# Performance work log

Measured on AMD Instinct MI355X. Metric: run time of the kernel, lower is better.

## Reference

```python
import jax, jax.numpy as jnp
import numpy as np

NUM_HEADS = 12

def setup_inputs() -> dict:
    key = jax.random.key(0)
    k1, k2, k3 = jax.random.split(key, 3)
    B, T, H = 2, 2048, 768
    x = jax.random.normal(k1, (B, T, H), dtype=jnp.float32)
    attn_mask = jnp.ones((B, T), dtype=jnp.int32)
    Wqkv = jax.random.normal(k2, (H, 3 * H), dtype=jnp.float32) * 0.02
    bqkv = jnp.zeros((3 * H,), dtype=jnp.float32)
    Wproj = jax.random.normal(k3, (H, H), dtype=jnp.float32) * 0.02
    bproj = jnp.zeros((H,), dtype=jnp.float32)
    return {"x": x, "attn_mask": attn_mask, "Wqkv": Wqkv, "bqkv": bqkv,
            "Wproj": Wproj, "bproj": bproj}

def reference(x, attn_mask, Wqkv, bqkv, Wproj, bproj):
    B, T, H = x.shape
    nh = NUM_HEADS
    hd = H // nh
    qkv = x @ Wqkv + bqkv                      # [B,T,3H]
    q, k, v = jnp.split(qkv, 3, axis=-1)
    # [B,T,H] -> [B,nh,T,hd]
    def heads(t):
        return t.reshape(B, T, nh, hd).transpose(0, 2, 1, 3)
    q, k, v = heads(q), heads(k), heads(v)
    scores = jnp.einsum('bhqd,bhkd->bhqk', q, k) / jnp.sqrt(jnp.float32(hd))
    causal = jnp.tril(jnp.ones((T, T), dtype=bool))          # allowed positions
    key_ok = attn_mask.astype(bool)[:, None, None, :]        # [B,1,1,T]
    allowed = causal[None, None] & key_ok
    scores = jnp.where(allowed, scores, -jnp.inf)
    weights = jax.nn.softmax(scores, axis=-1)                # dropout=0 (eval)
    out = jnp.einsum('bhqk,bhkd->bhqd', weights, v)
    out = out.transpose(0, 2, 1, 3).reshape(B, T, H)
    return out @ Wproj + bproj
```

## Files before the change

### kernel.cpp

```cpp
#include <hip/hip_runtime.h>
#include <stdint.h>

typedef unsigned short u16;
typedef unsigned int   u32;
typedef unsigned char  u8;
typedef __attribute__((ext_vector_type(8))) short short8;
typedef __attribute__((ext_vector_type(4))) float f32x4;
typedef __attribute__((ext_vector_type(4))) unsigned short u16x4;
typedef __attribute__((ext_vector_type(4))) unsigned int u32x4;

#define DEV static __device__ __forceinline__

static constexpr int Bc = 2, Tc = 2048, Hc = 768, NH = 12, HD = 64;
static constexpr int BTc = Bc * Tc;
static constexpr int N3 = 3 * Hc;
static constexpr int NBH = Bc * NH;
static constexpr int NITEMS = 32 * NBH;
static constexpr float QSCALE = 0.125f * 1.44269504088896f;
static constexpr float MRINIT = -1.0e38f;
static constexpr float SMASK  = -3.0e38f;

DEV u16 f2bf(float f) {
  u32 u = __float_as_uint(f);
  u32 r = (u + 0x7fffu + ((u >> 16) & 1u)) >> 16;
  return (u16)r;
}

DEV float fexp2(float x) {
#if __has_builtin(__builtin_amdgcn_exp2f)
  return __builtin_amdgcn_exp2f(x);
#else
  return exp2f(x);
#endif
}

DEV u32 cvtpk_bf16(float lo, float hi) {
  u32 r;
  asm("v_cvt_pk_bf16_f32 %0, %1, %2" : "=v"(r) : "v"(lo), "v"(hi));
  return r;
}

DEV void gl_lds16(const u16* g, u16* l) {
  __builtin_amdgcn_global_load_lds(
      (const __attribute__((address_space(1))) u32*)g,
      (__attribute__((address_space(3))) u32*)l, 16, 0, 0);
}

#define MFMA(a, b, c) __builtin_amdgcn_mfma_f32_16x16x32_bf16((a), (b), (c), 0, 0, 0)

__global__ void k_cvt(const float4* __restrict__ in, uint4* __restrict__ out, int n8,
                      const int* __restrict__ mask, u8* __restrict__ flags,
                      u32* __restrict__ ctr) {
  if (blockIdx.x == 0 && threadIdx.x < 64) {
    int t = threadIdx.x;
    if (t == 0) *ctr = 0;
    int b = t >> 5, kb = t & 31;
    const int* m = mask + b * Tc + kb * 64;
    int all = 1;
    for (int i = 0; i < 64; ++i) all &= (m[i] != 0);
    flags[b * 32 + kb] = (u8)all;
  }
  int i = blockIdx.x * 256 + threadIdx.x;
  if (i >= n8) return;
  float4 a = in[2 * i], b = in[2 * i + 1];
  uint4 o;
  o.x = f2bf(a.x) | ((u32)f2bf(a.y) << 16);
  o.y = f2bf(a.z) | ((u32)f2bf(a.w) << 16);
  o.z = f2bf(b.x) | ((u32)f2bf(b.y) << 16);
  o.w = f2bf(b.z) | ((u32)f2bf(b.w) << 16);
  out[i] = o;
}

__global__ __launch_bounds__(256) void k_transpose_w2(const float* __restrict__ Wqkv,
                                                      const float* __restrict__ Wproj,
                                                      u16* __restrict__ WqkvT,
                                                      u16* __restrict__ WprojT) {
  __shared__ u16 tile[64][65];
  int y = blockIdx.y, x = blockIdx.x;
  const float* in; u16* out; int R, C, r0, c0;
  if (y < 12) { in = Wqkv; out = WqkvT; R = Hc; C = N3; r0 = y * 64; c0 = x * 64; }
  else {
    if (x >= 12) return;
    in = Wproj; out = WprojT; R = Hc; C = Hc; r0 = (y - 12) * 64; c0 = x * 64;
  }
  int tx = threadIdx.x, ty = threadIdx.y;
  for (int i = ty; i < 64; i += 4)
    tile[i][tx] = f2bf(in[(size_t)(r0 + i) * C + c0 + tx]);
  __syncthreads();
  for (int i = ty; i < 64; i += 4)
    out[(size_t)(c0 + i) * R + r0 + tx] = tile[tx][i];
}

template <int EPI>
__global__ __launch_bounds__(256) void k_gemm(const u16* __restrict__ A,
                                              const u16* __restrict__ BTm,
                                              const float* __restrict__ bias,
                                              u16* __restrict__ oQ, u16* __restrict__ oK,
                                              u16* __restrict__ oV, float* __restrict__ oF,
                                              int M, int N, int K) {
  __shared__ u16 As[128 * 32];
  __shared__ u16 Bs[128 * 32];
  const int tid = threadIdx.x;
  const int lane = tid & 63, wave = tid >> 6;
  const int wr = wave >> 1, wc = wave & 1;
  const int row0 = blockIdx.y * 128, col0 = blockIdx.x * 128;

  f32x4 acc[4][4];
#pragma unroll
  for (int m = 0; m < 4; ++m)
#pragma unroll
    for (int n = 0; n < 4; ++n) acc[m][n] = (f32x4)(0.f);

  const int srow = lane >> 2;
  const int sg = lane & 3;
  const int sf = (lane >> 3) & 3;
  const int kfetch = ((sg ^ sf) * 8);

  const int r16 = lane & 15;
  const int g = lane >> 4;
  const int fr = (r16 >> 1) & 3;
  const int koff = ((g ^ fr) * 8);

  for (int k0 = 0; k0 < K; k0 += 32) {
    if (k0) __syncthreads();
#pragma unroll
    for (int p = 0; p < 2; ++p) {
      int seg = wave * 2 + p;
      int row = seg * 16 + srow;
      gl_lds16(A + (size_t)(row0 + row) * K + k0 + kfetch, &As[seg * 512 + lane * 8]);
      gl_lds16(BTm + (size_t)(col0 + row) * K + k0 + kfetch, &Bs[seg * 512 + lane * 8]);
    }
    __syncthreads();
    short8 af[4], bf[4];
#pragma unroll
    for (int m = 0; m < 4; ++m)
      af[m] = *(const short8*)&As[(wr * 64 + m * 16 + r16) * 32 + koff];
#pragma unroll
    for (int n = 0; n < 4; ++n)
      bf[n] = *(const short8*)&Bs[(wc * 64 + n * 16 + r16) * 32 + koff];
#pragma unroll
    for (int m = 0; m < 4; ++m)
#pragma unroll
      for (int n = 0; n < 4; ++n)
        acc[m][n] = MFMA(af[m], bf[n], acc[m][n]);
  }

#pragma unroll
  for (int m = 0; m < 4; ++m) {
    int rowg = row0 + wr * 64 + m * 16 + g * 4;
#pragma unroll
    for (int n = 0; n < 4; ++n) {
      int colg = col0 + wc * 64 + n * 16 + r16;
      float bv = bias[colg];
      if constexpr (EPI == 0) {
        int which = colg / Hc;
        int hc = colg - which * Hc;
        int h = hc >> 6, d = hc & 63;
        int b = rowg >> 11, t0 = rowg & 2047;
        if (which == 2) {
          int o = t0 & 31;
          int t0p = (t0 & ~31) | (((o >> 2) & 3) * 8 + ((o >> 4) & 1) * 4);
          u16x4 pk;
#pragma unroll
          for (int r = 0; r < 4; ++r) pk[r] = f2bf(acc[m][n][r] + bv);
          *(u16x4*)&oV[((size_t)(b * NH + h) * HD + d) * Tc + t0p] = pk;
        } else {
#pragma unroll
          for (int r = 0; r < 4; ++r) {
            float v = acc[m][n][r] + bv;
            size_t dst = ((size_t)(b * NH + h) * Tc + t0 + r) * HD + d;
            if (which == 0) oQ[dst] = f2bf(v * QSCALE);
            else            oK[dst] = f2bf(v);
          }
        }
      } else {
#pragma unroll
        for (int r = 0; r < 4; ++r)
          oF[(size_t)(rowg + r) * Hc + colg] = acc[m][n][r] + bv;
      }
    }
  }
}

__global__ __launch_bounds__(512, 4) void k_attn(const u16* __restrict__ Qh,
                                                 const u16* __restrict__ Kh,
                                                 const u16* __restrict__ VT,
                                                 const int* __restrict__ mask,
                                                 const u8* __restrict__ flags,
                                                 u16* __restrict__ O,
                                                 u32* __restrict__ ctr) {
  __shared__ u16 Ks[4][4096];
  __shared__ u16 Vs[4][4096];
  __shared__ float mlb[128];
  __shared__ int s_item;
  const int tid = threadIdx.x, lane = tid & 63, wave = tid >> 6;
  const int qgrp = wave >> 1;
  const int kh = wave & 1;
  const int r16 = lane & 15, g = lane >> 4;
  const int r7 = r16 & 7;
  const int skey = lane >> 3;
  const int sgr = lane & 7;
  const int sgd = ((sgr ^ skey) * 8);

  const int off0 = r16 * 64 + ((g ^ r7) * 8);
  const int off1 = r16 * 64 + (((4 + g) ^ r7) * 8);
  const int offv = kh ? off1 : off0;

  for (;;) {
    if (tid == 0) s_item = (int)atomicAdd(ctr, 1u);
    __syncthreads();
    const int item = s_item;
    if (item >= NITEMS) break;
    const int qt = 31 - item / NBH;
    const int bh = item % NBH;
    const int b = bh / NH, h = bh - b * NH;
    const int q0 = qt * 64;
    const int nt = qt + 1;
    const int qg = q0 + qgrp * 16 + r16;
    const int* mrow = mask + b * Tc;
    const u8* frow = flags + b * 32;

    const u16* qbase = Qh + ((size_t)bh * Tc + qg) * HD;
    const short8 qf0 = *(const short8*)(qbase + g * 8);
    const short8 qf1 = *(const short8*)(qbase + 32 + g * 8);

    f32x4 acc[4];
#pragma unroll
    for (int n = 0; n < 4; ++n) acc[n] = (f32x4)(0.f);
    float mrun = MRINIT, lrun = 0.f;

    const u16* kgb = Kh + (size_t)bh * Tc * HD;
    const u16* vgb = VT + (size_t)bh * HD * Tc;

    auto stage = [&](int slot, int kb) {
      int rloc = wave * 8 + skey;
      gl_lds16(kgb + (size_t)(kb + rloc) * HD + sgd, &Ks[slot][wave * 512 + lane * 8]);
      gl_lds16(vgb + (size_t)rloc * Tc + kb + sgd, &Vs[slot][wave * 512 + lane * 8]);
    };

    f32x4 sP0, sP1;
    auto process = [&](int u, f32x4 s0, f32x4 s1) {
      const int kbw = 64 * u + 32 * kh;
      const bool diag = (u == nt - 1);
      if (diag || !frow[u]) {
        const int fl = frow[u];
#pragma unroll
        for (int np = 0; np < 2; ++np)
#pragma unroll
          for (int r = 0; r < 4; ++r) {
            int keyg = kbw + 16 * np + 4 * g + r;
            bool ok = fl ? true : (mrow[keyg] != 0);
            if (diag) ok = ok && (keyg <= qg);
            if (!ok) { if (np == 0) s0[r] = SMASK; else s1[r] = SMASK; }
          }
      }
      float lm = fmaxf(fmaxf(fmaxf(s0[0], s0[1]), fmaxf(s0[2], s0[3])),
                       fmaxf(fmaxf(s1[0], s1[1]), fmaxf(s1[2], s1[3])));
      if (!__all(lm <= mrun + 8.0f)) {
        float rm = fmaxf(lm, __shfl_xor(lm, 16));
        rm = fmaxf(rm, __shfl_xor(rm, 32));
        float nm = fmaxf(mrun, rm);
        float alpha = fexp2(mrun - nm);
        mrun = nm;
        lrun *= alpha;
#pragma unroll
        for (int r = 0; r < 4; ++r) {
          float ar = __shfl(alpha, g * 4 + r);
          acc[0][r] *= ar; acc[1][r] *= ar; acc[2][r] *= ar; acc[3][r] *= ar;
        }
      }
      float p0[4], p1[4];
#pragma unroll
      for (int r = 0; r < 4; ++r) {
        p0[r] = fexp2(s0[r] - mrun);
        p1[r] = fexp2(s1[r] - mrun);
      }
      lrun += ((p0[0] + p0[1]) + (p0[2] + p0[3])) + ((p1[0] + p1[1]) + (p1[2] + p1[3]));
      u32x4 PL;
      PL[0] = cvtpk_bf16(p0[0], p0[1]); PL[1] = cvtpk_bf16(p0[2], p0[3]);
      PL[2] = cvtpk_bf16(p1[0], p1[1]); PL[3] = cvtpk_bf16(p1[2], p1[3]);
      short8 pa = __builtin_bit_cast(short8, PL);
      const u16* Vc = &Vs[u & 3][0];
      __builtin_amdgcn_s_setprio(1);
#pragma unroll
      for (int n = 0; n < 4; ++n) {
        short8 vf = *(const short8*)&Vc[n * 1024 + offv];
        acc[n] = MFMA(pa, vf, acc[n]);
      }
      __builtin_amdgcn_s_setprio(0);
    };

    stage(0, 0);
    if (nt > 1) stage(1, 64);

    for (int t = 0; t < nt; ++t) {
      const int kb = t * 64;
      const int rem = nt - 1 - t;

      if (rem >= 1) asm volatile("s_waitcnt vmcnt(2)" ::: "memory");
      else          asm volatile("s_waitcnt vmcnt(0)" ::: "memory");
      __builtin_amdgcn_sched_barrier(0);
      __builtin_amdgcn_s_barrier();
      __builtin_amdgcn_sched_barrier(0);

      if (rem >= 2) stage((t + 2) & 3, kb + 128);

      const u16* Kc = &Ks[t & 3][0];
      f32x4 sN0, sN1;
      __builtin_amdgcn_s_setprio(1);
      {
        const int ng = 2 * kh;
        short8 kf0 = *(const short8*)&Kc[ng * 1024 + off0];
        short8 kf1 = *(const short8*)&Kc[ng * 1024 + off1];
        f32x4 z = (f32x4)(0.f);
        z = MFMA(kf0, qf0, z); z = MFMA(kf1, qf1, z);
        sN0 = z;
        short8 kf2 = *(const short8*)&Kc[(ng + 1) * 1024 + off0];
        short8 kf3 = *(const short8*)&Kc[(ng + 1) * 1024 + off1];
        f32x4 w = (f32x4)(0.f);
        w = MFMA(kf2, qf0, w); w = MFMA(kf3, qf1, w);
        sN1 = w;
      }
      __builtin_amdgcn_s_setprio(0);

      if (t > 0) process(t - 1, sP0, sP1);
      sP0 = sN0; sP1 = sN1;
    }
    process(nt - 1, sP0, sP1);

    float lt = lrun + __shfl_xor(lrun, 16);
    lt += __shfl_xor(lt, 32);

    __syncthreads();
    float* ab = (float*)&Ks[0][0] + qgrp * 1024;
    if (kh == 1) {
#pragma unroll
      for (int n = 0; n < 4; ++n)
#pragma unroll
        for (int r = 0; r < 4; ++r)
          ab[(4 * g + r) * 64 + 16 * n + r16] = acc[n][r];
      if (g == 0) {
        mlb[qgrp * 32 + r16 * 2]     = mrun;
        mlb[qgrp * 32 + r16 * 2 + 1] = lt;
      }
    }
    __syncthreads();
    if (kh == 0) {
#pragma unroll
      for (int r = 0; r < 4; ++r) {
        int q = 4 * g + r;
        float mA = __shfl(mrun, q);
        float lA = __shfl(lt, q);
        float mB = mlb[qgrp * 32 + q * 2];
        float lB = mlb[qgrp * 32 + q * 2 + 1];
        float ms = fmaxf(mA, mB);
        float cA = fexp2(mA - ms);
        float cB = fexp2(mB - ms);
        float linv = 1.0f / (lA * cA + lB * cB);
        int qr = q0 + qgrp * 16 + q;
        u16* orow = O + ((size_t)(b * Tc + qr)) * Hc + h * 64;
#pragma unroll
        for (int n = 0; n < 4; ++n) {
          float v = (acc[n][r] * cA + ab[q * 64 + 16 * n + r16] * cB) * linv;
          orow[n * 16 + r16] = f2bf(v);
        }
      }
    }
  }
}

extern "C" void kernel_launch(void* const* d_in, const int* in_sizes, int n_in,
                              void* d_out, int out_size, void* d_ws, size_t ws_size,
                              hipStream_t stream) {
  const float* x = (const float*)d_in[0];
  const int* mask = (const int*)d_in[1];
  const float* Wqkv = (const float*)d_in[2];
  const float* bqkv = (const float*)d_in[3];
  const float* Wproj = (const float*)d_in[4];
  const float* bproj = (const float*)d_in[5];
  float* out = (float*)d_out;

  char* ws = (char*)d_ws;
  size_t off = 0;
  auto alloc = [&](size_t bytes) {
    char* p = ws + off;
    off += (bytes + 255) & ~(size_t)255;
    return p;
  };
  u16* xb     = (u16*)alloc((size_t)BTc * Hc * 2);
  u16* WqkvT  = (u16*)alloc((size_t)N3 * Hc * 2);
  u16* WprojT = (u16*)alloc((size_t)Hc * Hc * 2);
  u16* Qh     = (u16*)alloc((size_t)BTc * Hc * 2);
  u16* Kh     = (u16*)alloc((size_t)BTc * Hc * 2);
  u16* VT     = (u16*)alloc((size_t)BTc * Hc * 2);
  u32* ctr    = (u32*)alloc(256);
  u8*  flags  = (u8*)alloc(256);
  u16* Ob     = xb;

  int n8 = BTc * Hc / 8;
  k_cvt<<<(n8 + 255) / 256, 256, 0, stream>>>((const float4*)x, (uint4*)xb, n8,
                                              mask, flags, ctr);
  k_transpose_w2<<<dim3(36, 24), dim3(64, 4), 0, stream>>>(Wqkv, Wproj, WqkvT, WprojT);
  k_gemm<0><<<dim3(N3 / 128, BTc / 128), 256, 0, stream>>>(xb, WqkvT, bqkv, Qh, Kh, VT,
                                                           nullptr, BTc, N3, Hc);
  k_attn<<<dim3(512), 512, 0, stream>>>(Qh, Kh, VT, mask, flags, Ob, ctr);
  k_gemm<1><<<dim3(Hc / 128, BTc / 128), 256, 0, stream>>>(Ob, WprojT, bproj, nullptr,
                                                           nullptr, nullptr, out, BTc, Hc, Hc);
}
```

Baseline: 103.6 us.

## Triple-buffer GEMM loads with XCD swizzle; simplify attention to double-buffered loop

The GEMM kernel gains a three-slot LDS ring with prefetch two K-steps ahead and a single barrier per step, replacing the load/sync/compute loop. It also remaps workgroup IDs in an XCD-aware interleave to improve L2 locality. The attention kernel drops its software-pipelined QK/PV overlap and four-slot K/V ring in favour of a simpler two-slot loop with a full vmcnt(0) wait, removes the setprio hints, and launches NITEMS blocks instead of 512. This cuts attention LDS use, which may raise occupancy, but loses the overlap of QK^T with softmax/PV and exposes load latency.

After: 106.7 us. +3.0%, slower.

```diff
diff --git a/kernel.cpp b/kernel.cpp
--- a/kernel.cpp
+++ b/kernel.cpp
@@ -98,12 +98,17 @@
                                               u16* __restrict__ oQ, u16* __restrict__ oK,
                                               u16* __restrict__ oV, float* __restrict__ oF,
                                               int M, int N, int K) {
-  __shared__ u16 As[128 * 32];
-  __shared__ u16 Bs[128 * 32];
+  __shared__ u16 As[3][4096];
+  __shared__ u16 Bs[3][4096];
   const int tid = threadIdx.x;
   const int lane = tid & 63, wave = tid >> 6;
   const int wr = wave >> 1, wc = wave & 1;
-  const int row0 = blockIdx.y * 128, col0 = blockIdx.x * 128;
+
+  const int gx = gridDim.x;
+  const int nwg = gx * gridDim.y;
+  const int lin = blockIdx.y * gx + blockIdx.x;
+  const int wg = (lin & 7) * (nwg >> 3) + (lin >> 3);
+  const int row0 = (wg / gx) * 128, col0 = (wg % gx) * 128;
 
   f32x4 acc[4][4];
 #pragma unroll
@@ -121,23 +126,37 @@
   const int fr = (r16 >> 1) & 3;
   const int koff = ((g ^ fr) * 8);
 
-  for (int k0 = 0; k0 < K; k0 += 32) {
-    if (k0) __syncthreads();
+  auto stageG = [&](int slot, int k0) {
 #pragma unroll
     for (int p = 0; p < 2; ++p) {
       int seg = wave * 2 + p;
       int row = seg * 16 + srow;
-      gl_lds16(A + (size_t)(row0 + row) * K + k0 + kfetch, &As[seg * 512 + lane * 8]);
-      gl_lds16(BTm + (size_t)(col0 + row) * K + k0 + kfetch, &Bs[seg * 512 + lane * 8]);
+      gl_lds16(A + (size_t)(row0 + row) * K + k0 + kfetch, &As[slot][seg * 512 + lane * 8]);
+      gl_lds16(BTm + (size_t)(col0 + row) * K + k0 + kfetch, &Bs[slot][seg * 512 + lane * 8]);
     }
-    __syncthreads();
+  };
+
+  const int nk = K >> 5;
+  stageG(0, 0);
+  if (nk > 1) stageG(1, 32);
+
+  for (int kt = 0; kt < nk; ++kt) {
+    if (kt + 1 < nk) asm volatile("s_waitcnt vmcnt(4)" ::: "memory");
+    else             asm volatile("s_waitcnt vmcnt(0)" ::: "memory");
+    __builtin_amdgcn_sched_barrier(0);
+    __builtin_amdgcn_s_barrier();
+    __builtin_amdgcn_sched_barrier(0);
+    if (kt + 2 < nk) stageG((kt + 2) % 3, (kt + 2) * 32);
+
+    const u16* Ac = &As[kt % 3][0];
+    const u16* Bcur = &Bs[kt % 3][0];
     short8 af[4], bf[4];
 #pragma unroll
     for (int m = 0; m < 4; ++m)
-      af[m] = *(const short8*)&As[(wr * 64 + m * 16 + r16) * 32 + koff];
+      af[m] = *(const short8*)&Ac[(wr * 64 + m * 16 + r16) * 32 + koff];
 #pragma unroll
     for (int n = 0; n < 4; ++n)
-      bf[n] = *(const short8*)&Bs[(wc * 64 + n * 16 + r16) * 32 + koff];
+      bf[n] = *(const short8*)&Bcur[(wc * 64 + n * 16 + r16) * 32 + koff];
 #pragma unroll
     for (int m = 0; m < 4; ++m)
 #pragma unroll
@@ -189,8 +208,8 @@
                                                  const u8* __restrict__ flags,
                                                  u16* __restrict__ O,
                                                  u32* __restrict__ ctr) {
-  __shared__ u16 Ks[4][4096];
-  __shared__ u16 Vs[4][4096];
+  __shared__ u16 Ks[2][4096];
+  __shared__ u16 Vs[2][4096];
   __shared__ float mlb[128];
   __shared__ int s_item;
   const int tid = threadIdx.x, lane = tid & 63, wave = tid >> 6;
@@ -238,12 +257,40 @@
       gl_lds16(vgb + (size_t)rloc * Tc + kb + sgd, &Vs[slot][wave * 512 + lane * 8]);
     };
 
-    f32x4 sP0, sP1;
-    auto process = [&](int u, f32x4 s0, f32x4 s1) {
-      const int kbw = 64 * u + 32 * kh;
-      const bool diag = (u == nt - 1);
-      if (diag || !frow[u]) {
-        const int fl = frow[u];
+    stage(0, 0);
+
+    for (int t = 0; t < nt; ++t) {
+      const int kb = t * 64;
+
+      asm volatile("s_waitcnt vmcnt(0)" ::: "memory");
+      __builtin_amdgcn_sched_barrier(0);
+      __builtin_amdgcn_s_barrier();
+      __builtin_amdgcn_sched_barrier(0);
+
+      if (t + 1 < nt) stage((t + 1) & 1, kb + 64);
+
+      const u16* Kc = &Ks[t & 1][0];
+      const u16* Vc = &Vs[t & 1][0];
+
+      f32x4 s0, s1;
+      {
+        const int ng = 2 * kh;
+        short8 kf0 = *(const short8*)&Kc[ng * 1024 + off0];
+        short8 kf1 = *(const short8*)&Kc[ng * 1024 + off1];
+        f32x4 z = (f32x4)(0.f);
+        z = MFMA(kf0, qf0, z); z = MFMA(kf1, qf1, z);
+        s0 = z;
+        short8 kf2 = *(const short8*)&Kc[(ng + 1) * 1024 + off0];
+        short8 kf3 = *(const short8*)&Kc[(ng + 1) * 1024 + off1];
+        f32x4 w = (f32x4)(0.f);
+        w = MFMA(kf2, qf0, w); w = MFMA(kf3, qf1, w);
+        s1 = w;
+      }
+
+      const int kbw = kb + 32 * kh;
+      const bool diag = (t == nt - 1);
+      if (diag || !frow[t]) {
+        const int fl = frow[t];
 #pragma unroll
         for (int np = 0; np < 2; ++np)
 #pragma unroll
@@ -254,6 +301,7 @@
             if (!ok) { if (np == 0) s0[r] = SMASK; else s1[r] = SMASK; }
           }
       }
+
       float lm = fmaxf(fmaxf(fmaxf(s0[0], s0[1]), fmaxf(s0[2], s0[3])),
                        fmaxf(fmaxf(s1[0], s1[1]), fmaxf(s1[2], s1[3])));
       if (!__all(lm <= mrun + 8.0f)) {
@@ -276,57 +324,18 @@
         p1[r] = fexp2(s1[r] - mrun);
       }
       lrun += ((p0[0] + p0[1]) + (p0[2] + p0[3])) + ((p1[0] + p1[1]) + (p1[2] + p1[3]));
+
       u32x4 PL;
       PL[0] = cvtpk_bf16(p0[0], p0[1]); PL[1] = cvtpk_bf16(p0[2], p0[3]);
       PL[2] = cvtpk_bf16(p1[0], p1[1]); PL[3] = cvtpk_bf16(p1[2], p1[3]);
       short8 pa = __builtin_bit_cast(short8, PL);
-      const u16* Vc = &Vs[u & 3][0];
-      __builtin_amdgcn_s_setprio(1);
 #pragma unroll
       for (int n = 0; n < 4; ++n) {
         short8 vf = *(const short8*)&Vc[n * 1024 + offv];
         acc[n] = MFMA(pa, vf, acc[n]);
       }
-      __builtin_amdgcn_s_setprio(0);
-    };
-
-    stage(0, 0);
-    if (nt > 1) stage(1, 64);
-
-    for (int t = 0; t < nt; ++t) {
-      const int kb = t * 64;
-      const int rem = nt - 1 - t;
-
-      if (rem >= 1) asm volatile("s_waitcnt vmcnt(2)" ::: "memory");
-      else          asm volatile("s_waitcnt vmcnt(0)" ::: "memory");
       __builtin_amdgcn_sched_barrier(0);
-      __builtin_amdgcn_s_barrier();
-      __builtin_amdgcn_sched_barrier(0);
-
-      if (rem >= 2) stage((t + 2) & 3, kb + 128);
-
-      const u16* Kc = &Ks[t & 3][0];
-      f32x4 sN0, sN1;
-      __builtin_amdgcn_s_setprio(1);
-      {
-        const int ng = 2 * kh;
-        short8 kf0 = *(const short8*)&Kc[ng * 1024 + off0];
-        short8 kf1 = *(const short8*)&Kc[ng * 1024 + off1];
-        f32x4 z = (f32x4)(0.f);
-        z = MFMA(kf0, qf0, z); z = MFMA(kf1, qf1, z);
-        sN0 = z;
-        short8 kf2 = *(const short8*)&Kc[(ng + 1) * 1024 + off0];
-        short8 kf3 = *(const short8*)&Kc[(ng + 1) * 1024 + off1];
-        f32x4 w = (f32x4)(0.f);
-        w = MFMA(kf2, qf0, w); w = MFMA(kf3, qf1, w);
-        sN1 = w;
-      }
-      __builtin_amdgcn_s_setprio(0);
-
-      if (t > 0) process(t - 1, sP0, sP1);
-      sP0 = sN0; sP1 = sN1;
     }
-    process(nt - 1, sP0, sP1);
 
     float lt = lrun + __shfl_xor(lrun, 16);
     lt += __shfl_xor(lt, 32);
@@ -403,7 +412,7 @@
   k_transpose_w2<<<dim3(36, 24), dim3(64, 4), 0, stream>>>(Wqkv, Wproj, WqkvT, WprojT);
   k_gemm<0><<<dim3(N3 / 128, BTc / 128), 256, 0, stream>>>(xb, WqkvT, bqkv, Qh, Kh, VT,
                                                            nullptr, BTc, N3, Hc);
-  k_attn<<<dim3(512), 512, 0, stream>>>(Qh, Kh, VT, mask, flags, Ob, ctr);
+  k_attn<<<dim3(NITEMS), 512, 0, stream>>>(Qh, Kh, VT, mask, flags, Ob, ctr);
   k_gemm<1><<<dim3(Hc / 128, BTc / 128), 256, 0, stream>>>(Ob, WprojT, bproj, nullptr,
                                                            nullptr, nullptr, out, BTc, Hc, Hc);
 }
```
